# Kernel tuning notes

Hardware: AMD Instinct MI355X
Metric: run time of the kernel (lower is better)

## Reference

```python
import jax, jax.numpy as jnp
import numpy as np

HIDDEN = 2048
FFN = 4096
E = 16
TOPK = 4


def setup_inputs() -> dict:
    key = jax.random.key(0)
    ks = jax.random.split(key, 5)
    scale = 0.02
    x = jax.random.normal(ks[0], (1, 2048, HIDDEN), dtype=jnp.float32)
    router_w = jax.random.normal(ks[1], (E, HIDDEN), dtype=jnp.float32) * scale  # nn.Linear weight [out,in]
    w1 = jax.random.normal(ks[2], (E, HIDDEN, FFN), dtype=jnp.float32) * scale
    v1 = jax.random.normal(ks[3], (E, HIDDEN, FFN), dtype=jnp.float32) * scale
    w2 = jax.random.normal(ks[4], (E, FFN, HIDDEN), dtype=jnp.float32) * scale
    return {"x": x, "router_w": router_w, "w1": w1, "v1": v1, "w2": w2}


def reference(x, router_w, w1, v1, w2):
    B, S, H = x.shape
    xf = x.reshape(-1, H)                       # [T, H]
    T = xf.shape[0]
    # Router: softmax in fp32, then top-k
    logits = xf @ router_w.T                    # [T, E]
    weights = jax.nn.softmax(logits.astype(jnp.float32), axis=-1)
    top_w, top_e = jax.lax.top_k(weights, TOPK)  # [T, K]
    # moe_normalize_expert_weights = 1.0 -> L1 normalize
    top_w = top_w / jnp.sum(jnp.abs(top_w), axis=-1, keepdims=True)
    weights = weights.astype(x.dtype)
    top_w = top_w.astype(x.dtype)
    # Dense combine matrix [T, E]: sum of top-k weights per expert slot
    combine = jnp.zeros((T, E), dtype=x.dtype)
    combine = combine.at[jnp.arange(T)[:, None], top_e].add(top_w)
    # Per-expert gated MLP, vectorized over experts
    h = jnp.einsum('th,ehf->etf', xf, w1)       # [E, T, F]
    v = jnp.einsum('th,ehf->etf', xf, v1)       # [E, T, F]
    y = jnp.einsum('etf,efh->eth', jax.nn.silu(h) * v, w2)  # [E, T, H]
    out = jnp.einsum('eth,te->th', y, combine).reshape(B, S, H)
    return out, weights
```

## Files before the change

kernel.cpp:

```cpp
#include <hip/hip_runtime.h>
#include <hip/hip_bf16.h>
#include <cstdint>

#define HID 2048
#define FFN 4096
#define NE 16
#define NTOK 2048
#define TOPK 4
#define BM 256
#define BN 64
#define BK 64
#define MAXT 48
#define TOTROWS 8192
#define GRID1 (MAXT * (FFN / BN))
#define GRID2 (MAXT * (HID / BN))
#define CHUNK1 (GRID1 / 8)
#define CHUNK2 (GRID2 / 8)

typedef __attribute__((ext_vector_type(4))) float f32x4;
typedef __attribute__((ext_vector_type(8))) short bf16x8;

__device__ __forceinline__ ushort f2bf(float f) {
  __hip_bfloat16 h = __float2bfloat16(f);
  return *reinterpret_cast<ushort*>(&h);
}

__device__ __forceinline__ int swz(int row) { return (row ^ (row >> 2)) & 7; }

__device__ __forceinline__ void gload_lds16(const void* g, void* l) {
  __builtin_amdgcn_global_load_lds((const __attribute__((address_space(1))) void*)g,
                                   (__attribute__((address_space(3))) void*)l, 16, 0, 0);
}

__global__ void init_kernel(int* __restrict__ counts) {
  if (threadIdx.x < NE) counts[threadIdx.x] = 0;
}

__global__ void cvt_x_kernel(const float* __restrict__ x, ushort* __restrict__ xbf) {
  int i = blockIdx.x * 256 + threadIdx.x;
  float4 v = ((const float4*)x)[i];
  ushort4 o;
  o.x = f2bf(v.x); o.y = f2bf(v.y); o.z = f2bf(v.z); o.w = f2bf(v.w);
  ((ushort4*)xbf)[i] = o;
}

__global__ void router_kernel(const float* __restrict__ x, const float* __restrict__ rw,
                              float* __restrict__ wout, float* __restrict__ combine,
                              int* __restrict__ counts) {
  int t = blockIdx.x;
  int tid = threadIdx.x, lane = tid & 63, w = tid >> 6;
  const float* xr = x + (size_t)t * HID;
  const float* r0 = rw + (size_t)(w * 4 + 0) * HID;
  const float* r1 = rw + (size_t)(w * 4 + 1) * HID;
  const float* r2 = rw + (size_t)(w * 4 + 2) * HID;
  const float* r3 = rw + (size_t)(w * 4 + 3) * HID;
  float s0 = 0.f, s1 = 0.f, s2 = 0.f, s3 = 0.f;
  for (int h = lane; h < HID; h += 64) {
    float xv = xr[h];
    s0 += xv * r0[h]; s1 += xv * r1[h]; s2 += xv * r2[h]; s3 += xv * r3[h];
  }
  #pragma unroll
  for (int off = 32; off > 0; off >>= 1) {
    s0 += __shfl_down(s0, off); s1 += __shfl_down(s1, off);
    s2 += __shfl_down(s2, off); s3 += __shfl_down(s3, off);
  }
  __shared__ float logits[NE];
  if (lane == 0) {
    logits[w * 4 + 0] = s0; logits[w * 4 + 1] = s1;
    logits[w * 4 + 2] = s2; logits[w * 4 + 3] = s3;
  }
  __syncthreads();
  if (tid == 0) {
    float p[NE];
    float mx = logits[0];
    #pragma unroll
    for (int e = 1; e < NE; e++) mx = fmaxf(mx, logits[e]);
    float ssum = 0.f;
    #pragma unroll
    for (int e = 0; e < NE; e++) { p[e] = expf(logits[e] - mx); ssum += p[e]; }
    float inv = 1.0f / ssum;
    #pragma unroll
    for (int e = 0; e < NE; e++) { p[e] *= inv; wout[t * NE + e] = p[e]; }
    int sel[TOPK]; float selw[TOPK];
    unsigned used = 0;
    for (int k = 0; k < TOPK; k++) {
      int best = 0; float bw = -1.0f;
      for (int e = 0; e < NE; e++)
        if (!((used >> e) & 1u) && p[e] > bw) { bw = p[e]; best = e; }
      used |= 1u << best; sel[k] = best; selw[k] = bw;
    }
    float sw = selw[0] + selw[1] + selw[2] + selw[3];
    float invs = 1.0f / sw;
    float comb[NE];
    #pragma unroll
    for (int e = 0; e < NE; e++) comb[e] = 0.f;
    for (int k = 0; k < TOPK; k++) comb[sel[k]] = selw[k] * invs;
    #pragma unroll
    for (int e = 0; e < NE; e++) combine[t * NE + e] = comb[e];
    for (int k = 0; k < TOPK; k++) atomicAdd(&counts[sel[k]], 1);
  }
}

__global__ void build_tiles_kernel(const int* __restrict__ counts, int* __restrict__ seg_off,
                                   int* __restrict__ tiles, int* __restrict__ ntiles) {
  if (blockIdx.x != 0 || threadIdx.x != 0) return;
  int off = 0, nt = 0;
  for (int e = 0; e < NE; e++) {
    seg_off[e] = off;
    int c = counts[e];
    for (int rb = 0; rb * BM < c; rb++) {
      tiles[nt * 3 + 0] = e;
      tiles[nt * 3 + 1] = off + rb * BM;
      tiles[nt * 3 + 2] = (c - rb * BM < BM) ? (c - rb * BM) : BM;
      nt++;
    }
    off += c;
  }
  seg_off[NE] = off;
  *ntiles = nt;
}

__global__ void assign_kernel(const float* __restrict__ combine, const int* __restrict__ seg_off,
                              int* __restrict__ token_flat, float* __restrict__ gate_flat) {
  int e = blockIdx.x;
  int tid = threadIdx.x, lane = tid & 63, w = tid >> 6;
  __shared__ int base;
  __shared__ int wtot[4];
  if (tid == 0) base = seg_off[e];
  __syncthreads();
  for (int t0 = 0; t0 < NTOK; t0 += 256) {
    int t = t0 + tid;
    float g = combine[t * NE + e];
    int flag = (g > 0.0f) ? 1 : 0;
    unsigned long long m = __ballot(flag);
    if (lane == 0) wtot[w] = __popcll(m);
    __syncthreads();
    int pre = 0;
    for (int j = 0; j < w; j++) pre += wtot[j];
    int tot = wtot[0] + wtot[1] + wtot[2] + wtot[3];
    int lp = __popcll(m & ((1ull << lane) - 1ull));
    if (flag) {
      int pos = base + pre + lp;
      token_flat[pos] = t;
      gate_flat[pos] = g;
    }
    __syncthreads();
    if (tid == 0) base += tot;
    __syncthreads();
  }
}

__global__ __launch_bounds__(512, 4) void mlp1_kernel(
    const ushort* __restrict__ xbf, const float* __restrict__ w1, const float* __restrict__ v1,
    const int* __restrict__ tiles, const int* __restrict__ ntiles,
    const int* __restrict__ token_flat, ushort* __restrict__ G) {
  int id = blockIdx.x;
  int wg = (id & 7) * CHUNK1 + (id >> 3);
  int tile = wg % MAXT, nblk = wg / MAXT;
  if (tile >= *ntiles) return;
  const int e  = tiles[tile * 3 + 0];
  const int g0 = tiles[tile * 3 + 1];
  const int nr = tiles[tile * 3 + 2];
  const int n0 = nblk * BN;

  __shared__ __align__(16) ushort As[2][BM * BK];
  __shared__ __align__(16) ushort Bw[BN * BK];
  __shared__ __align__(16) ushort Bv[BN * BK];

  const int tid = threadIdx.x, lane = tid & 63, wv = tid >> 6;
  const int wr = wv >> 1, wc = wv & 1;
  const int fr = lane & 15, fq = lane >> 4;

  uint aoff[4];
  int aslot[4];
  #pragma unroll
  for (int i = 0; i < 4; i++) {
    int slot = i * 512 + tid;
    int m = slot >> 3, g = slot & 7;
    int r = m < nr ? m : (nr - 1);
    int tok = token_flat[g0 + r];
    aoff[i] = (uint)(tok * HID + ((g ^ swz(m)) << 3));
    aslot[i] = slot * 8;
  }

  const int bs = tid & 255;
  const int bnq = bs & 15, bkq = bs >> 4;
  const float* bsrc = ((tid >> 8) ? v1 : w1) + (size_t)e * HID * FFN + (size_t)(bkq * 4) * FFN + n0 + bnq * 4;
  ushort* bdst = (tid >> 8) ? Bv : Bw;
  uint boff[4];
  #pragma unroll
  for (int c = 0; c < 4; c++) {
    int n = bnq * 4 + c;
    boff[c] = (uint)(n * 128 + (((bkq >> 1) ^ swz(n)) << 4) + ((bkq & 1) << 3));
  }

  float4 br0, br1, br2, br3;
  #define LOADB(k0) { size_t kb = (size_t)(k0) * FFN; \
      br0 = *(const float4*)(bsrc + kb); br1 = *(const float4*)(bsrc + kb + FFN); \
      br2 = *(const float4*)(bsrc + kb + 2 * FFN); br3 = *(const float4*)(bsrc + kb + 3 * FFN); }
  #define WRITEB() { const float* rr[4] = {(const float*)&br0, (const float*)&br1, (const float*)&br2, (const float*)&br3}; \
      _Pragma("unroll") for (int c = 0; c < 4; c++) { \
        union { ushort u[4]; uint2 v; } p; \
        _Pragma("unroll") for (int j = 0; j < 4; j++) p.u[j] = f2bf(rr[j][c]); \
        *(uint2*)((char*)bdst + boff[c]) = p.v; } }

  LOADB(0);
  #pragma unroll
  for (int i = 0; i < 4; i++)
    gload_lds16(xbf + aoff[i], &As[0][aslot[i]]);
  WRITEB();
  __syncthreads();

  f32x4 acc_h[4][2] = {};
  f32x4 acc_v[4][2] = {};
  int cur = 0;

  for (int t = 0; t < HID / BK; t++) {
    const int last = (t == HID / BK - 1);
    if (!last) {
      int kn = (t + 1) * BK;
      LOADB(kn);
      ushort* abase = &As[cur ^ 1][0];
      #pragma unroll
      for (int i = 0; i < 4; i++)
        gload_lds16(xbf + aoff[i] + kn, abase + aslot[i]);
    }
    const char* Ab = (const char*)&As[cur][0];
    #pragma unroll
    for (int hk = 0; hk < 2; hk++) {
      bf16x8 af[4], bwf[2], bvf[2];
      #pragma unroll
      for (int am = 0; am < 4; am++) {
        int m = wr * 64 + am * 16 + fr;
        af[am] = *(const bf16x8*)(Ab + m * 128 + (((hk * 4 + fq) ^ swz(m)) << 4));
      }
      #pragma unroll
      for (int an = 0; an < 2; an++) {
        int n = wc * 32 + an * 16 + fr;
        int off = n * 128 + (((hk * 4 + fq) ^ swz(n)) << 4);
        bwf[an] = *(const bf16x8*)((const char*)Bw + off);
        bvf[an] = *(const bf16x8*)((const char*)Bv + off);
      }
      #pragma unroll
      for (int am = 0; am < 4; am++)
        #pragma unroll
        for (int an = 0; an < 2; an++) {
          acc_h[am][an] = __builtin_amdgcn_mfma_f32_16x16x32_bf16(af[am], bwf[an], acc_h[am][an], 0, 0, 0);
          acc_v[am][an] = __builtin_amdgcn_mfma_f32_16x16x32_bf16(af[am], bvf[an], acc_v[am][an], 0, 0, 0);
        }
    }
    __syncthreads();
    if (!last) { WRITEB(); }
    __syncthreads();
    cur ^= 1;
  }

  #pragma unroll
  for (int am = 0; am < 4; am++) {
    #pragma unroll
    for (int j = 0; j < 4; j++) {
      int m = wr * 64 + am * 16 + fq * 4 + j;
      if (m < nr) {
        ushort* grow = G + (size_t)(g0 + m) * FFN + n0 + wc * 32 + fr;
        #pragma unroll
        for (int an = 0; an < 2; an++) {
          float h = acc_h[am][an][j];
          float v = acc_v[am][an][j];
          float g = h / (1.0f + __expf(-h)) * v;
          grow[an * 16] = f2bf(g);
        }
      }
    }
  }
  #undef LOADB
  #undef WRITEB
}

__global__ __launch_bounds__(512, 4) void mlp2_kernel(
    const ushort* __restrict__ G, const float* __restrict__ w2,
    const int* __restrict__ tiles, const int* __restrict__ ntiles,
    const int* __restrict__ token_flat, const float* __restrict__ gate_flat,
    float* __restrict__ out) {
  int id = blockIdx.x;
  int wg = (id & 7) * CHUNK2 + (id >> 3);
  int tile = wg % MAXT, nblk = wg / MAXT;
  if (tile >= *ntiles) return;
  const int e  = tiles[tile * 3 + 0];
  const int g0 = tiles[tile * 3 + 1];
  const int nr = tiles[tile * 3 + 2];
  const int n0 = nblk * BN;

  __shared__ __align__(16) ushort As[2][BM * BK];
  __shared__ __align__(16) ushort Bs[BN * BK];

  const int tid = threadIdx.x, lane = tid & 63, wv = tid >> 6;
  const int wr = wv >> 1, wc = wv & 1;
  const int fr = lane & 15, fq = lane >> 4;

  uint aoff[4];
  int aslot[4];
  #pragma unroll
  for (int i = 0; i < 4; i++) {
    int slot = i * 512 + tid;
    int m = slot >> 3, g = slot & 7;
    int r = m < nr ? m : (nr - 1);
    aoff[i] = (uint)((g0 + r) * FFN + ((g ^ swz(m)) << 3));
    aslot[i] = slot * 8;
  }

  const int bnq = tid & 15, bkq2 = tid >> 4;
  const float* bsrc = w2 + (size_t)e * FFN * HID + (size_t)(bkq2 * 2) * HID + n0 + bnq * 4;
  uint boff[4];
  #pragma unroll
  for (int c = 0; c < 4; c++) {
    int n = bnq * 4 + c;
    int k = bkq2 * 2;
    boff[c] = (uint)(n * 128 + (((k >> 3) ^ swz(n)) << 4) + ((k & 7) << 1));
  }

  float4 br0, br1;
  #define LOADB2(k0) { size_t kb = (size_t)(k0) * HID; \
      br0 = *(const float4*)(bsrc + kb); br1 = *(const float4*)(bsrc + kb + HID); }
  #define WRITEB2() { const float* rr[2] = {(const float*)&br0, (const float*)&br1}; \
      _Pragma("unroll") for (int c = 0; c < 4; c++) { \
        union { ushort u[2]; uint v; } p; \
        p.u[0] = f2bf(rr[0][c]); p.u[1] = f2bf(rr[1][c]); \
        *(uint*)((char*)Bs + boff[c]) = p.v; } }

  LOADB2(0);
  #pragma unroll
  for (int i = 0; i < 4; i++)
    gload_lds16(G + aoff[i], &As[0][aslot[i]]);
  WRITEB2();
  __syncthreads();

  f32x4 acc[4][2] = {};
  int cur = 0;

  for (int t = 0; t < FFN / BK; t++) {
    const int last = (t == FFN / BK - 1);
    if (!last) {
      int kn = (t + 1) * BK;
      LOADB2(kn);
      ushort* abase = &As[cur ^ 1][0];
      #pragma unroll
      for (int i = 0; i < 4; i++)
        gload_lds16(G + aoff[i] + kn, abase + aslot[i]);
    }
    const char* Ab = (const char*)&As[cur][0];
    #pragma unroll
    for (int hk = 0; hk < 2; hk++) {
      bf16x8 af[4], bf_[2];
      #pragma unroll
      for (int am = 0; am < 4; am++) {
        int m = wr * 64 + am * 16 + fr;
        af[am] = *(const bf16x8*)(Ab + m * 128 + (((hk * 4 + fq) ^ swz(m)) << 4));
      }
      #pragma unroll
      for (int an = 0; an < 2; an++) {
        int n = wc * 32 + an * 16 + fr;
        bf_[an] = *(const bf16x8*)((const char*)Bs + n * 128 + (((hk * 4 + fq) ^ swz(n)) << 4));
      }
      #pragma unroll
      for (int am = 0; am < 4; am++)
        #pragma unroll
        for (int an = 0; an < 2; an++)
          acc[am][an] = __builtin_amdgcn_mfma_f32_16x16x32_bf16(af[am], bf_[an], acc[am][an], 0, 0, 0);
    }
    __syncthreads();
    if (!last) { WRITEB2(); }
    __syncthreads();
    cur ^= 1;
  }

  #pragma unroll
  for (int am = 0; am < 4; am++) {
    #pragma unroll
    for (int j = 0; j < 4; j++) {
      int m = wr * 64 + am * 16 + fq * 4 + j;
      if (m < nr) {
        float gate = gate_flat[g0 + m];
        int tok = token_flat[g0 + m];
        float* orow = out + (size_t)tok * HID + n0 + wc * 32 + fr;
        #pragma unroll
        for (int an = 0; an < 2; an++)
          atomicAdd(&orow[an * 16], acc[am][an][j] * gate);
      }
    }
  }
  #undef LOADB2
  #undef WRITEB2
}

extern "C" void kernel_launch(void* const* d_in, const int* in_sizes, int n_in,
                              void* d_out, int out_size, void* d_ws, size_t ws_size,
                              hipStream_t stream) {
  const float* x  = (const float*)d_in[0];
  const float* rw = (const float*)d_in[1];
  const float* w1 = (const float*)d_in[2];
  const float* v1 = (const float*)d_in[3];
  const float* w2 = (const float*)d_in[4];
  float* out0 = (float*)d_out;
  float* wout = out0 + (size_t)NTOK * HID;

  char* ws = (char*)d_ws;
  float* combine    = (float*)(ws + 0);
  int*   counts     = (int*)(ws + 131072);
  int*   seg_off    = (int*)(ws + 131200);
  int*   ntiles     = (int*)(ws + 131328);
  int*   tiles      = (int*)(ws + 131392);
  int*   token_flat = (int*)(ws + 132352);
  float* gate_flat  = (float*)(ws + 165120);
  ushort* G         = (ushort*)(ws + 262144);
  ushort* xbf       = (ushort*)(ws + 262144 + (size_t)TOTROWS * FFN * 2);

  hipMemsetAsync(d_out, 0, (size_t)out_size * sizeof(float), stream);
  init_kernel<<<1, 64, 0, stream>>>(counts);
  cvt_x_kernel<<<(NTOK * HID / 4) / 256, 256, 0, stream>>>(x, (ushort*)xbf);
  router_kernel<<<NTOK, 256, 0, stream>>>(x, rw, wout, combine, counts);
  build_tiles_kernel<<<1, 1, 0, stream>>>(counts, seg_off, tiles, ntiles);
  assign_kernel<<<NE, 256, 0, stream>>>(combine, seg_off, token_flat, gate_flat);
  mlp1_kernel<<<GRID1, 512, 0, stream>>>(xbf, w1, v1, tiles, ntiles, token_flat, G);
  mlp2_kernel<<<GRID2, 512, 0, stream>>>(G, w2, tiles, ntiles, token_flat, gate_flat, out0);
}
```

Baseline: 989.7 us.

## Replace atomic scatter-add in down-projection with bf16 scratch plus gather-combine kernel

The down-projection kernel now writes gate-scaled results per routed row into a bf16 scratch buffer instead of doing fp32 atomicAdds into the output. A new per-token combine kernel gathers each token's top-k rows through a position map built in assign_kernel and sums them. This also removes the output memset. It avoids atomic contention and read-modify-write traffic, at the cost of an extra kernel, the scratch write and read, bf16 rounding of the partial results, and tok_pos entries that are never initialized if a token has fewer than TOPK nonzero slots.

```diff
diff --git a/kernel.cpp b/kernel.cpp
--- a/kernel.cpp
+++ b/kernel.cpp
@@ -25,6 +25,11 @@
   return *reinterpret_cast<ushort*>(&h);
 }
 
+__device__ __forceinline__ float bf2f(ushort u) {
+  unsigned int v = ((unsigned int)u) << 16;
+  return *reinterpret_cast<float*>(&v);
+}
+
 __device__ __forceinline__ int swz(int row) { return (row ^ (row >> 2)) & 7; }
 
 __device__ __forceinline__ void gload_lds16(const void* g, void* l) {
@@ -121,7 +126,8 @@
 }
 
 __global__ void assign_kernel(const float* __restrict__ combine, const int* __restrict__ seg_off,
-                              int* __restrict__ token_flat, float* __restrict__ gate_flat) {
+                              int* __restrict__ token_flat, float* __restrict__ gate_flat,
+                              int* __restrict__ tok_pos) {
   int e = blockIdx.x;
   int tid = threadIdx.x, lane = tid & 63, w = tid >> 6;
   __shared__ int base;
@@ -143,6 +149,9 @@
       int pos = base + pre + lp;
       token_flat[pos] = t;
       gate_flat[pos] = g;
+      int slot = 0;
+      for (int e2 = 0; e2 < e; e2++) slot += (combine[t * NE + e2] > 0.0f) ? 1 : 0;
+      if (slot < TOPK) tok_pos[t * TOPK + slot] = pos;
     }
     __syncthreads();
     if (tid == 0) base += tot;
@@ -279,8 +288,7 @@
 __global__ __launch_bounds__(512, 4) void mlp2_kernel(
     const ushort* __restrict__ G, const float* __restrict__ w2,
     const int* __restrict__ tiles, const int* __restrict__ ntiles,
-    const int* __restrict__ token_flat, const float* __restrict__ gate_flat,
-    float* __restrict__ out) {
+    const float* __restrict__ gate_flat, ushort* __restrict__ yscr) {
   int id = blockIdx.x;
   int wg = (id & 7) * CHUNK2 + (id >> 3);
   int tile = wg % MAXT, nblk = wg / MAXT;
@@ -380,16 +388,36 @@
       int m = wr * 64 + am * 16 + fq * 4 + j;
       if (m < nr) {
         float gate = gate_flat[g0 + m];
-        int tok = token_flat[g0 + m];
-        float* orow = out + (size_t)tok * HID + n0 + wc * 32 + fr;
+        ushort* yrow = yscr + (size_t)(g0 + m) * HID + n0 + wc * 32 + fr;
         #pragma unroll
         for (int an = 0; an < 2; an++)
-          atomicAdd(&orow[an * 16], acc[am][an][j] * gate);
+          yrow[an * 16] = f2bf(acc[am][an][j] * gate);
       }
     }
   }
   #undef LOADB2
   #undef WRITEB2
+}
+
+__global__ void combine_kernel(const ushort* __restrict__ yscr, const int* __restrict__ tok_pos,
+                               float* __restrict__ out) {
+  int t = blockIdx.x, tid = threadIdx.x;
+  int c0 = tid * 8;
+  float s[8] = {0.f, 0.f, 0.f, 0.f, 0.f, 0.f, 0.f, 0.f};
+  #pragma unroll
+  for (int k = 0; k < TOPK; k++) {
+    int pos = tok_pos[t * TOPK + k];
+    if (pos >= 0 && pos < TOTROWS) {
+      const ushort4* yr = (const ushort4*)(yscr + (size_t)pos * HID + c0);
+      ushort4 a = yr[0], b = yr[1];
+      s[0] += bf2f(a.x); s[1] += bf2f(a.y); s[2] += bf2f(a.z); s[3] += bf2f(a.w);
+      s[4] += bf2f(b.x); s[5] += bf2f(b.y); s[6] += bf2f(b.z); s[7] += bf2f(b.w);
+    }
+  }
+  float4* op = (float4*)(out + (size_t)t * HID + c0);
+  float4 o0 = {s[0], s[1], s[2], s[3]};
+  float4 o1 = {s[4], s[5], s[6], s[7]};
+  op[0] = o0; op[1] = o1;
 }
 
 extern "C" void kernel_launch(void* const* d_in, const int* in_sizes, int n_in,
@@ -411,15 +439,18 @@
   int*   tiles      = (int*)(ws + 131392);
   int*   token_flat = (int*)(ws + 132352);
   float* gate_flat  = (float*)(ws + 165120);
+  int*   tok_pos    = (int*)(ws + 197888);
   ushort* G         = (ushort*)(ws + 262144);
   ushort* xbf       = (ushort*)(ws + 262144 + (size_t)TOTROWS * FFN * 2);
-
-  hipMemsetAsync(d_out, 0, (size_t)out_size * sizeof(float), stream);
+  ushort* yscr      = (ushort*)(ws + 262144 + (size_t)TOTROWS * FFN * 2
+                                 + (size_t)NTOK * HID * 2);
+
   init_kernel<<<1, 64, 0, stream>>>(counts);
   cvt_x_kernel<<<(NTOK * HID / 4) / 256, 256, 0, stream>>>(x, (ushort*)xbf);
   router_kernel<<<NTOK, 256, 0, stream>>>(x, rw, wout, combine, counts);
   build_tiles_kernel<<<1, 1, 0, stream>>>(counts, seg_off, tiles, ntiles);
-  assign_kernel<<<NE, 256, 0, stream>>>(combine, seg_off, token_flat, gate_flat);
+  assign_kernel<<<NE, 256, 0, stream>>>(combine, seg_off, token_flat, gate_flat, tok_pos);
   mlp1_kernel<<<GRID1, 512, 0, stream>>>(xbf, w1, v1, tiles, ntiles, token_flat, G);
-  mlp2_kernel<<<GRID2, 512, 0, stream>>>(G, w2, tiles, ntiles, token_flat, gate_flat, out0);
-}
+  mlp2_kernel<<<GRID2, 512, 0, stream>>>(G, w2, tiles, ntiles, gate_flat, yscr);
+  combine_kernel<<<NTOK, 256, 0, stream>>>(yscr, tok_pos, out0);
+}
```

Result: no change. 989.2 us (-0.0%).
